# Optimization experiments

Measured on AMD Instinct MI355X. Metric: run time of the kernel, lower is better.

Reference implementation:

```python
import jax, jax.numpy as jnp
import numpy as np

N = 50000

def _norm_coeffs(edge_index, n):
    # add self-loops, compute symmetric GCN normalization D^-1/2 (A+I) D^-1/2
    loops = jnp.arange(n, dtype=edge_index.dtype)
    src = jnp.concatenate([edge_index[0], loops])
    dst = jnp.concatenate([edge_index[1], loops])
    deg = jax.ops.segment_sum(jnp.ones_like(dst, dtype=jnp.float32), dst, num_segments=n)
    dinv = jnp.where(deg > 0, jax.lax.rsqrt(deg), 0.0)
    norm = dinv[src] * dinv[dst]  # [E+N]
    return src, dst, norm

def _gcn(x, W, b, src, dst, norm, n):
    h = x @ W                                   # [N, out]
    m = h[src] * norm[:, None]                  # [E+N, out] gather + scale
    return jax.ops.segment_sum(m, dst, num_segments=n) + b

def setup_inputs() -> dict:
    key = jax.random.key(0)
    ks = jax.random.split(key, 8)
    d, h = 96, 96
    E = 800000
    return {
        "x": jax.random.normal(ks[0], (N, d), jnp.float32),
        "edge_index": jax.random.randint(ks[1], (2, E), 0, N, dtype=jnp.int64),
        "h_prev": jax.random.normal(ks[2], (N, h), jnp.float32),
        "Wx": jax.random.normal(ks[3], (d, h), jnp.float32) * (1.0 / np.sqrt(d)),
        "bx": jnp.zeros((h,), jnp.float32),
        "Wuh": jax.random.normal(ks[4], (2 * h, h), jnp.float32) * (1.0 / np.sqrt(2 * h)),
        "buh": jnp.zeros((h,), jnp.float32),
        "Wch": jax.random.normal(ks[5], (2 * h, h), jnp.float32) * (1.0 / np.sqrt(2 * h)),
        "bch": jnp.zeros((h,), jnp.float32),
    }

def reference(x, edge_index, h_prev, Wx, bx, Wuh, buh, Wch, bch):
    n = x.shape[0]
    src, dst, norm = _norm_coeffs(edge_index, n)
    x_gcn = _gcn(x, Wx, bx, src, dst, norm, n)
    combined = jnp.concatenate([x_gcn, h_prev], axis=1)
    # original computes gcn_uh(combined) twice for u and r; identical math -> compute once
    g = jax.nn.sigmoid(_gcn(combined, Wuh, buh, src, dst, norm, n))
    u = g
    r = g
    combined_r = jnp.concatenate([x_gcn, r * h_prev], axis=1)
    c = jnp.tanh(_gcn(combined_r, Wch, bch, src, dst, norm, n))
    return u * h_prev + (1.0 - u) * c
```

## Files before the change

kernel.cpp:

```cpp
#include <hip/hip_runtime.h>
#include <hip/hip_bf16.h>

#define D 96
#define CAP 64
typedef long long i64;
typedef unsigned short u16;

typedef __bf16 bf16x8 __attribute__((ext_vector_type(8)));
typedef float f32x16 __attribute__((ext_vector_type(16)));

__device__ __forceinline__ float bf2f(u16 u) {
  union { unsigned u; float f; } x; x.u = ((unsigned)u) << 16; return x.f;
}
__device__ __forceinline__ void unpack8(uint4 p, float* a) {
  a[0] = bf2f((u16)(p.x & 0xffff)); a[1] = bf2f((u16)(p.x >> 16));
  a[2] = bf2f((u16)(p.y & 0xffff)); a[3] = bf2f((u16)(p.y >> 16));
  a[4] = bf2f((u16)(p.z & 0xffff)); a[5] = bf2f((u16)(p.z >> 16));
  a[6] = bf2f((u16)(p.w & 0xffff)); a[7] = bf2f((u16)(p.w >> 16));
}

__device__ __forceinline__ void split8(const float* v8, bf16x8& hi, bf16x8& lo) {
  unsigned hu[4], lu[4];
#pragma unroll
  for (int p = 0; p < 4; p++) {
    float v0 = v8[2 * p], v1 = v8[2 * p + 1];
    unsigned u0 = __float_as_uint(v0), u1 = __float_as_uint(v1);
    hu[p] = (u0 >> 16) | (u1 & 0xffff0000u);
    float l0 = v0 - __uint_as_float(u0 & 0xffff0000u);
    float l1 = v1 - __uint_as_float(u1 & 0xffff0000u);
    lu[p] = (__float_as_uint(l0) >> 16) | (__float_as_uint(l1) & 0xffff0000u);
  }
  union { uint4 q; bf16x8 v; } H, L;
  H.q = make_uint4(hu[0], hu[1], hu[2], hu[3]);
  L.q = make_uint4(lu[0], lu[1], lu[2], lu[3]);
  hi = H.v; lo = L.v;
}

__global__ __launch_bounds__(256) void k_detect(const unsigned* __restrict__ w,
                                                int* flag, int E) {
  if (threadIdx.x < 64) {
    int lane = threadIdx.x;
    int lim = (E < 2048) ? E : 2048;
    unsigned acc = 0;
    for (int j = lane; j < lim; j += 64) acc |= w[2 * j + 1];
#pragma unroll
    for (int off = 32; off > 0; off >>= 1) acc |= __shfl_down(acc, off, 64);
    if (lane == 0) *flag = (acc == 0) ? 1 : 0;
  }
}

__global__ __launch_bounds__(256) void k_wprep(const float* __restrict__ Wx,
                                               const float* __restrict__ Wuh,
                                               const float* __restrict__ Wch,
                                               u16* __restrict__ wxh, u16* __restrict__ wxl,
                                               u16* __restrict__ wuhh, u16* __restrict__ wuhl,
                                               u16* __restrict__ wchh, u16* __restrict__ wchl) {
  int cid = blockIdx.x * 256 + threadIdx.x;
  const float* W; u16 *oh, *ol; int loc;
  if (cid < 1152) { W = Wx; oh = wxh; ol = wxl; loc = cid; }
  else if (cid < 3456) { W = Wuh; oh = wuhh; ol = wuhl; loc = cid - 1152; }
  else if (cid < 5760) { W = Wch; oh = wchh; ol = wchl; loc = cid - 3456; }
  else return;
  int oct = loc / 96;
  int j = loc - oct * 96;
  int k0 = oct * 8;
  unsigned hu[4], lu[4];
#pragma unroll
  for (int p = 0; p < 4; p++) {
    float v0 = W[(size_t)(k0 + 2 * p) * D + j];
    float v1 = W[(size_t)(k0 + 2 * p + 1) * D + j];
    unsigned u0 = __float_as_uint(v0), u1 = __float_as_uint(v1);
    hu[p] = (u0 >> 16) | (u1 & 0xffff0000u);
    float l0 = v0 - __uint_as_float(u0 & 0xffff0000u);
    float l1 = v1 - __uint_as_float(u1 & 0xffff0000u);
    lu[p] = (__float_as_uint(l0) >> 16) | (__float_as_uint(l1) & 0xffff0000u);
  }
  *(uint4*)&oh[(size_t)loc * 8] = make_uint4(hu[0], hu[1], hu[2], hu[3]);
  *(uint4*)&ol[(size_t)loc * 8] = make_uint4(lu[0], lu[1], lu[2], lu[3]);
}

__global__ __launch_bounds__(256) void k_bucket(const int* __restrict__ e32,
                                                const i64* __restrict__ e64,
                                                const int* __restrict__ flagp,
                                                uint2* __restrict__ region,
                                                int* __restrict__ cntmat,
                                                int E, int N, int NB) {
  __shared__ int lofs[256];
  const int tid = threadIdx.x;
  const int blk = blockIdx.x;
  lofs[tid] = 0;
  __syncthreads();
  const int f = *flagp;
  const int chunk = (E + gridDim.x - 1) / gridDim.x;
  const int lo = blk * chunk;
  const int hi = min(E, lo + chunk);
  for (int i = lo + tid; i < hi; i += 256) {
    int d, s;
    if (f) { d = (int)e64[(size_t)E + i]; s = (int)e64[i]; }
    else   { d = e32[(size_t)E + i];      s = e32[i]; }
    if ((unsigned)d >= (unsigned)N || (unsigned)s >= (unsigned)N) continue;
    int q = d >> 8;
    int r = atomicAdd(&lofs[q], 1);
    if (r < CAP)
      region[((size_t)q * 256 + blk) * CAP + r] = make_uint2((unsigned)s, (unsigned)d);
  }
  __syncthreads();
  if (tid < NB) cntmat[blk * 256 + tid] = min(lofs[tid], CAP);
}

__global__ __launch_bounds__(256) void k_csr(const uint2* __restrict__ region,
                                             const int* __restrict__ cntmat,
                                             int* __restrict__ deg,
                                             int* __restrict__ csrp, int NB) {
  __shared__ int ldeg[256];
  __shared__ int lcsr[256 * CAP];
  const int tid = threadIdx.x;
  const int b = blockIdx.x;
  ldeg[tid] = 0;
  __syncthreads();
  int cnt = cntmat[tid * 256 + b];
  const uint2* cell = region + ((size_t)b * 256 + tid) * CAP;
  for (int k = 0; k < cnt; k++) {
    uint2 e = cell[k];
    int node = (int)(e.y & 255u);
    int r = atomicAdd(&ldeg[node], 1);
    if (r < CAP) lcsr[node * CAP + r] = (int)e.x;
  }
  __syncthreads();
  deg[(b << 8) + tid] = ldeg[tid];
  const uint4* src = (const uint4*)lcsr;
  uint4* dst = (uint4*)(csrp + ((size_t)b << 8) * CAP);
#pragma unroll
  for (int it = 0; it < (256 * CAP) / 4 / 256; it++)
    dst[tid + it * 256] = src[tid + it * 256];
}

template <int KTOT, int MODE>
__global__ __launch_bounds__(256) void gemm_mfma(
    const float* __restrict__ xin, const float* __restrict__ xg,
    const float* __restrict__ hprev, const float* __restrict__ gmul,
    const u16* __restrict__ whi, const u16* __restrict__ wlo,
    const int* __restrict__ deg, __hip_bfloat16* __restrict__ t, int N) {
  const int l = threadIdx.x & 63;
  const int wave = threadIdx.x >> 6;
  const int lr = l & 31;
  const int kg = l >> 5;
  const int rb = blockIdx.x * 128 + wave * 32;
  const int row = rb + lr;
  const bool rok = row < N;
  constexpr int steps = KTOT / 16;

  f32x16 acc0, acc1, acc2;
#pragma unroll
  for (int i = 0; i < 16; i++) { acc0[i] = 0.f; acc1[i] = 0.f; acc2[i] = 0.f; }

  auto loadA = [&](int s, float4& va, float4& vb, float4& ga, float4& gb) {
    if (!rok) return;
    int k0 = s * 16 + kg * 8;
    if (MODE == 0) {
      const float* src = &xin[(size_t)row * D + k0];
      va = *(const float4*)src; vb = *(const float4*)(src + 4);
    } else if (s < 6) {
      const float* src = &xg[(size_t)row * D + k0];
      va = *(const float4*)src; vb = *(const float4*)(src + 4);
    } else {
      const float* src = &hprev[(size_t)row * D + (k0 - 96)];
      va = *(const float4*)src; vb = *(const float4*)(src + 4);
      if (MODE == 2) {
        const float* gs = &gmul[(size_t)row * D + (k0 - 96)];
        ga = *(const float4*)gs; gb = *(const float4*)(gs + 4);
      }
    }
  };

  auto computeS = [&](int s, float4 va, float4 vb, float4 ga, float4 gb) {
    if (MODE == 2 && s >= 6) {
      va.x *= ga.x; va.y *= ga.y; va.z *= ga.z; va.w *= ga.w;
      vb.x *= gb.x; vb.y *= gb.y; vb.z *= gb.z; vb.w *= gb.w;
    }
    float a8[8] = {va.x, va.y, va.z, va.w, vb.x, vb.y, vb.z, vb.w};
    bf16x8 ah, al;
    split8(a8, ah, al);
    const size_t wbase = ((size_t)(s * 2 + kg) * 96 + lr) * 8;
    union { uint4 q; bf16x8 v; } B0h, B1h, B2h, B0l, B1l, B2l;
    B0h.q = *(const uint4*)&whi[wbase];
    B1h.q = *(const uint4*)&whi[wbase + 32 * 8];
    B2h.q = *(const uint4*)&whi[wbase + 64 * 8];
    B0l.q = *(const uint4*)&wlo[wbase];
    B1l.q = *(const uint4*)&wlo[wbase + 32 * 8];
    B2l.q = *(const uint4*)&wlo[wbase + 64 * 8];
    acc0 = __builtin_amdgcn_mfma_f32_32x32x16_bf16(ah, B0h.v, acc0, 0, 0, 0);
    acc1 = __builtin_amdgcn_mfma_f32_32x32x16_bf16(ah, B1h.v, acc1, 0, 0, 0);
    acc2 = __builtin_amdgcn_mfma_f32_32x32x16_bf16(ah, B2h.v, acc2, 0, 0, 0);
    acc0 = __builtin_amdgcn_mfma_f32_32x32x16_bf16(al, B0h.v, acc0, 0, 0, 0);
    acc1 = __builtin_amdgcn_mfma_f32_32x32x16_bf16(al, B1h.v, acc1, 0, 0, 0);
    acc2 = __builtin_amdgcn_mfma_f32_32x32x16_bf16(al, B2h.v, acc2, 0, 0, 0);
    acc0 = __builtin_amdgcn_mfma_f32_32x32x16_bf16(ah, B0l.v, acc0, 0, 0, 0);
    acc1 = __builtin_amdgcn_mfma_f32_32x32x16_bf16(ah, B1l.v, acc1, 0, 0, 0);
    acc2 = __builtin_amdgcn_mfma_f32_32x32x16_bf16(ah, B2l.v, acc2, 0, 0, 0);
  };

  float4 z4 = make_float4(0.f, 0.f, 0.f, 0.f);
  float4 va0 = z4, vb0 = z4, ga0 = z4, gb0 = z4;
  float4 va1 = z4, vb1 = z4, ga1 = z4, gb1 = z4;
  loadA(0, va0, vb0, ga0, gb0);
  loadA(1, va1, vb1, ga1, gb1);
#pragma unroll 1
  for (int s = 0; s < steps; s += 2) {
    computeS(s, va0, vb0, ga0, gb0);
    if (s + 2 < steps) loadA(s + 2, va0, vb0, ga0, gb0);
    computeS(s + 1, va1, vb1, ga1, gb1);
    if (s + 3 < steps) loadA(s + 3, va1, vb1, ga1, gb1);
  }

  const int rbase = rb + 4 * kg;
#pragma unroll
  for (int r = 0; r < 16; r++) {
    int orow = rbase + (r & 3) + 8 * (r >> 2);
    if (orow >= N) continue;
    float dv = rsqrtf((float)deg[orow] + 1.0f);
    __hip_bfloat16* tp = &t[(size_t)orow * D];
    tp[lr]      = __float2bfloat16(acc0[r] * dv);
    tp[lr + 32] = __float2bfloat16(acc1[r] * dv);
    tp[lr + 64] = __float2bfloat16(acc2[r] * dv);
  }
}

template <int MODE>
__global__ __launch_bounds__(192) void gather_fin(
    const __hip_bfloat16* __restrict__ t, const int* __restrict__ deg,
    const int* __restrict__ csrp,
    const float* __restrict__ bias,
    const float* __restrict__ g, const float* __restrict__ hprev,
    float* __restrict__ outf, int N) {
  __shared__ int lidx[16 * 65];
  __shared__ int ldeg[16];
  const int tid = threadIdx.x;
  const int vbase = blockIdx.x * 16;
#pragma unroll
  for (int it = 0; it < 6; it++) {
    int i = tid + it * 192;
    if (i < 1024) {
      int n = i >> 6, j = i & 63;
      lidx[n * 65 + j] = csrp[((size_t)(vbase + n)) * CAP + j];
    }
  }
  if (tid < 16) ldeg[tid] = deg[vbase + tid];
  __syncthreads();
  const int n = tid / 12;
  const int c8 = tid - n * 12;
  const int v = vbase + n;
  if (v >= N) return;
  const uint4* t8 = (const uint4*)t;
  float acc[8];
  unpack8(t8[(size_t)v * 12 + c8], acc);
  int dv_i = ldeg[n];
  int nb = min(dv_i, CAP);
  const int* ip = &lidx[n * 65];
  int j = 0;
  for (; j + 8 <= nb; j += 8) {
    int s0 = ip[j],     s1 = ip[j + 1], s2 = ip[j + 2], s3 = ip[j + 3];
    int s4 = ip[j + 4], s5 = ip[j + 5], s6 = ip[j + 6], s7 = ip[j + 7];
    uint4 p0 = t8[(size_t)s0 * 12 + c8];
    uint4 p1 = t8[(size_t)s1 * 12 + c8];
    uint4 p2 = t8[(size_t)s2 * 12 + c8];
    uint4 p3 = t8[(size_t)s3 * 12 + c8];
    uint4 p4 = t8[(size_t)s4 * 12 + c8];
    uint4 p5 = t8[(size_t)s5 * 12 + c8];
    uint4 p6 = t8[(size_t)s6 * 12 + c8];
    uint4 p7 = t8[(size_t)s7 * 12 + c8];
    float a0[8], a1[8], a2[8], a3[8], a4[8], a5[8], a6[8], a7[8];
    unpack8(p0, a0); unpack8(p1, a1); unpack8(p2, a2); unpack8(p3, a3);
    unpack8(p4, a4); unpack8(p5, a5); unpack8(p6, a6); unpack8(p7, a7);
#pragma unroll
    for (int q = 0; q < 8; q++)
      acc[q] += ((a0[q] + a1[q]) + (a2[q] + a3[q])) + ((a4[q] + a5[q]) + (a6[q] + a7[q]));
  }
  for (; j + 4 <= nb; j += 4) {
    int s0 = ip[j], s1 = ip[j + 1], s2 = ip[j + 2], s3 = ip[j + 3];
    uint4 p0 = t8[(size_t)s0 * 12 + c8];
    uint4 p1 = t8[(size_t)s1 * 12 + c8];
    uint4 p2 = t8[(size_t)s2 * 12 + c8];
    uint4 p3 = t8[(size_t)s3 * 12 + c8];
    float a0[8], a1[8], a2[8], a3[8];
    unpack8(p0, a0); unpack8(p1, a1); unpack8(p2, a2); unpack8(p3, a3);
#pragma unroll
    for (int q = 0; q < 8; q++) acc[q] += (a0[q] + a1[q]) + (a2[q] + a3[q]);
  }
  for (; j < nb; j++) {
    int s = ip[j];
    float a0[8];
    unpack8(t8[(size_t)s * 12 + c8], a0);
#pragma unroll
    for (int q = 0; q < 8; q++) acc[q] += a0[q];
  }
  float dv = rsqrtf((float)dv_i + 1.0f);
  float4 bA = ((const float4*)bias)[c8 * 2];
  float4 bB = ((const float4*)bias)[c8 * 2 + 1];
  float z[8] = {dv * acc[0] + bA.x, dv * acc[1] + bA.y, dv * acc[2] + bA.z, dv * acc[3] + bA.w,
                dv * acc[4] + bB.x, dv * acc[5] + bB.y, dv * acc[6] + bB.z, dv * acc[7] + bB.w};
  const size_t oidx = (size_t)v * 12 + c8;
  float4 oA, oB;
  if (MODE == 1) {
    oA = make_float4(z[0], z[1], z[2], z[3]);
    oB = make_float4(z[4], z[5], z[6], z[7]);
  } else if (MODE == 2) {
    oA = make_float4(1.0f / (1.0f + expf(-z[0])), 1.0f / (1.0f + expf(-z[1])),
                     1.0f / (1.0f + expf(-z[2])), 1.0f / (1.0f + expf(-z[3])));
    oB = make_float4(1.0f / (1.0f + expf(-z[4])), 1.0f / (1.0f + expf(-z[5])),
                     1.0f / (1.0f + expf(-z[6])), 1.0f / (1.0f + expf(-z[7])));
  } else {
    float4 uA = ((const float4*)g)[oidx * 2], uB = ((const float4*)g)[oidx * 2 + 1];
    float4 hA = ((const float4*)hprev)[oidx * 2], hB = ((const float4*)hprev)[oidx * 2 + 1];
    oA = make_float4(uA.x * hA.x + (1.0f - uA.x) * tanhf(z[0]),
                     uA.y * hA.y + (1.0f - uA.y) * tanhf(z[1]),
                     uA.z * hA.z + (1.0f - uA.z) * tanhf(z[2]),
                     uA.w * hA.w + (1.0f - uA.w) * tanhf(z[3]));
    oB = make_float4(uB.x * hB.x + (1.0f - uB.x) * tanhf(z[4]),
                     uB.y * hB.y + (1.0f - uB.y) * tanhf(z[5]),
                     uB.z * hB.z + (1.0f - uB.z) * tanhf(z[6]),
                     uB.w * hB.w + (1.0f - uB.w) * tanhf(z[7]));
  }
  ((float4*)outf)[oidx * 2] = oA;
  ((float4*)outf)[oidx * 2 + 1] = oB;
}

extern "C" void kernel_launch(void* const* d_in, const int* in_sizes, int n_in,
                              void* d_out, int out_size, void* d_ws, size_t ws_size,
                              hipStream_t stream) {
  const float* x = (const float*)d_in[0];
  const int* ei32 = (const int*)d_in[1];
  const i64* ei64 = (const i64*)d_in[1];
  const unsigned* eiw = (const unsigned*)d_in[1];
  const float* hp = (const float*)d_in[2];
  const float* Wx = (const float*)d_in[3];
  const float* bx = (const float*)d_in[4];
  const float* Wuh = (const float*)d_in[5];
  const float* buh = (const float*)d_in[6];
  const float* Wch = (const float*)d_in[7];
  const float* bch = (const float*)d_in[8];
  float* out = (float*)d_out;

  const int N = in_sizes[0] / D;
  const int E = in_sizes[1] / 2;
  const size_t NF = (size_t)N * D;
  const int NB = (N + 255) >> 8;
  const int R = NB << 8;

  char* base = (char*)d_ws;
  int* flag = (int*)base;
  u16* wxh = (u16*)(base + 256);
  u16* wxl = wxh + 9216;
  u16* wuhh = wxl + 9216;
  u16* wuhl = wuhh + 18432;
  u16* wchh = wuhl + 18432;
  u16* wchl = wchh + 18432;
  int* deg = (int*)(wchl + 18432);
  int* cntmat = deg + R;
  uint2* region = (uint2*)(cntmat + 65536);
  int* csrp = (int*)(region + (size_t)NB * 256 * CAP);
  __hip_bfloat16* t = (__hip_bfloat16*)(csrp + (size_t)R * CAP);
  float* xg = (float*)((char*)t + NF * 2);
  float* g = xg + NF;

  const int gb = (N + 127) / 128;
  const int fb = (N + 15) / 16;

  k_detect<<<1, 256, 0, stream>>>(eiw, flag, E);
  k_wprep<<<23, 256, 0, stream>>>(Wx, Wuh, Wch, wxh, wxl, wuhh, wuhl, wchh, wchl);
  k_bucket<<<256, 256, 0, stream>>>(ei32, ei64, flag, region, cntmat, E, N, NB);
  k_csr<<<NB, 256, 0, stream>>>(region, cntmat, deg, csrp, NB);

  gemm_mfma<96, 0><<<gb, 256, 0, stream>>>(x, nullptr, nullptr, nullptr, wxh, wxl, deg, t, N);
  gather_fin<1><<<fb, 192, 0, stream>>>(t, deg, csrp, bx, nullptr, nullptr, xg, N);

  gemm_mfma<192, 1><<<gb, 256, 0, stream>>>(nullptr, xg, hp, nullptr, wuhh, wuhl, deg, t, N);
  gather_fin<2><<<fb, 192, 0, stream>>>(t, deg, csrp, buh, nullptr, nullptr, g, N);

  gemm_mfma<192, 2><<<gb, 256, 0, stream>>>(nullptr, xg, hp, g, wchh, wchl, deg, t, N);
  gather_fin<3><<<fb, 192, 0, stream>>>(t, deg, csrp, bch, g, hp, out, N);
}
```

Before: 294.5 us.

## Switch GEMM to 16x16x32 MFMA tiles with two-wave split-K reduction

The dense GEMM kernels move from 32x32x16 MFMA tiles to 16x16x32 MFMA tiles, so each wave covers 16 rows and all 96 output columns. For the K=192 GEMMs, the two waves of a 128-thread block each take half of K (x_gcn or h_prev) and combine partial sums through a small shared-memory buffer. For K=96, each wave handles its own 16 rows. This launches many more, smaller blocks to raise occupancy and spread memory traffic. In exchange it adds a barrier and LDS round trip, and each block reuses the weight loads less.

```diff
diff --git a/kernel.cpp b/kernel.cpp
--- a/kernel.cpp
+++ b/kernel.cpp
@@ -7,7 +7,7 @@
 typedef unsigned short u16;
 
 typedef __bf16 bf16x8 __attribute__((ext_vector_type(8)));
-typedef float f32x16 __attribute__((ext_vector_type(16)));
+typedef float f32x4 __attribute__((ext_vector_type(4)));
 
 __device__ __forceinline__ float bf2f(u16 u) {
   union { unsigned u; float f; } x; x.u = ((unsigned)u) << 16; return x.f;
@@ -136,93 +136,100 @@
 }
 
 template <int KTOT, int MODE>
-__global__ __launch_bounds__(256) void gemm_mfma(
+__global__ __launch_bounds__(128) void gemm_mfma(
     const float* __restrict__ xin, const float* __restrict__ xg,
     const float* __restrict__ hprev, const float* __restrict__ gmul,
     const u16* __restrict__ whi, const u16* __restrict__ wlo,
     const int* __restrict__ deg, __hip_bfloat16* __restrict__ t, int N) {
+  constexpr bool KS = (KTOT == 192);
+  __shared__ float lcomb[64][25];
   const int l = threadIdx.x & 63;
-  const int wave = threadIdx.x >> 6;
-  const int lr = l & 31;
-  const int kg = l >> 5;
-  const int rb = blockIdx.x * 128 + wave * 32;
-  const int row = rb + lr;
+  const int wv = threadIdx.x >> 6;
+  const int j16 = l & 15;
+  const int koct = l >> 4;
+  const int rb = KS ? blockIdx.x * 16 : blockIdx.x * 32 + wv * 16;
+  const int row = rb + j16;
   const bool rok = row < N;
-  constexpr int steps = KTOT / 16;
-
-  f32x16 acc0, acc1, acc2;
-#pragma unroll
-  for (int i = 0; i < 16; i++) { acc0[i] = 0.f; acc1[i] = 0.f; acc2[i] = 0.f; }
-
-  auto loadA = [&](int s, float4& va, float4& vb, float4& ga, float4& gb) {
-    if (!rok) return;
-    int k0 = s * 16 + kg * 8;
-    if (MODE == 0) {
-      const float* src = &xin[(size_t)row * D + k0];
-      va = *(const float4*)src; vb = *(const float4*)(src + 4);
-    } else if (s < 6) {
-      const float* src = &xg[(size_t)row * D + k0];
-      va = *(const float4*)src; vb = *(const float4*)(src + 4);
-    } else {
-      const float* src = &hprev[(size_t)row * D + (k0 - 96)];
-      va = *(const float4*)src; vb = *(const float4*)(src + 4);
-      if (MODE == 2) {
-        const float* gs = &gmul[(size_t)row * D + (k0 - 96)];
-        ga = *(const float4*)gs; gb = *(const float4*)(gs + 4);
+
+  f32x4 c0, c1, c2, c3, c4, c5;
+#pragma unroll
+  for (int i = 0; i < 4; i++) { c0[i] = 0.f; c1[i] = 0.f; c2[i] = 0.f;
+                                c3[i] = 0.f; c4[i] = 0.f; c5[i] = 0.f; }
+
+#define COLT(CT, ACC) do {                                                  \
+    union { uint4 q; bf16x8 v; } Bh, Bl;                                    \
+    const size_t wb = (so + (CT)*16 + j16) * 8;                             \
+    Bh.q = *(const uint4*)&whi[wb];                                         \
+    Bl.q = *(const uint4*)&wlo[wb];                                         \
+    ACC = __builtin_amdgcn_mfma_f32_16x16x32_bf16(ah, Bh.v, ACC, 0, 0, 0);  \
+    ACC = __builtin_amdgcn_mfma_f32_16x16x32_bf16(al, Bh.v, ACC, 0, 0, 0);  \
+    ACC = __builtin_amdgcn_mfma_f32_16x16x32_bf16(ah, Bl.v, ACC, 0, 0, 0);  \
+  } while (0)
+
+#pragma unroll
+  for (int ss = 0; ss < 3; ss++) {
+    const int s = KS ? (wv * 3 + ss) : ss;
+    float a8[8] = {0.f, 0.f, 0.f, 0.f, 0.f, 0.f, 0.f, 0.f};
+    if (rok) {
+      const int kb = ss * 32 + koct * 8;
+      const float* src;
+      if (MODE == 0) src = xin;
+      else if (!KS || wv == 0) src = xg;
+      else src = hprev;
+      float4 va = *(const float4*)&src[(size_t)row * D + kb];
+      float4 vb = *(const float4*)&src[(size_t)row * D + kb + 4];
+      if (MODE == 2 && KS && wv == 1) {
+        float4 ga = *(const float4*)&gmul[(size_t)row * D + kb];
+        float4 gb = *(const float4*)&gmul[(size_t)row * D + kb + 4];
+        va.x *= ga.x; va.y *= ga.y; va.z *= ga.z; va.w *= ga.w;
+        vb.x *= gb.x; vb.y *= gb.y; vb.z *= gb.z; vb.w *= gb.w;
+      }
+      a8[0] = va.x; a8[1] = va.y; a8[2] = va.z; a8[3] = va.w;
+      a8[4] = vb.x; a8[5] = vb.y; a8[6] = vb.z; a8[7] = vb.w;
+    }
+    bf16x8 ah, al;
+    split8(a8, ah, al);
+    const size_t so = (size_t)(s * 4 + koct) * 96;
+    COLT(0, c0); COLT(1, c1); COLT(2, c2);
+    COLT(3, c3); COLT(4, c4); COLT(5, c5);
+  }
+#undef COLT
+
+  if (KS) {
+    if (wv == 1) {
+#pragma unroll
+      for (int r = 0; r < 4; r++) {
+        lcomb[l][0 + r]  = c0[r]; lcomb[l][4 + r]  = c1[r];
+        lcomb[l][8 + r]  = c2[r]; lcomb[l][12 + r] = c3[r];
+        lcomb[l][16 + r] = c4[r]; lcomb[l][20 + r] = c5[r];
       }
     }
-  };
-
-  auto computeS = [&](int s, float4 va, float4 vb, float4 ga, float4 gb) {
-    if (MODE == 2 && s >= 6) {
-      va.x *= ga.x; va.y *= ga.y; va.z *= ga.z; va.w *= ga.w;
-      vb.x *= gb.x; vb.y *= gb.y; vb.z *= gb.z; vb.w *= gb.w;
+    __syncthreads();
+    if (wv == 1) return;
+#pragma unroll
+    for (int r = 0; r < 4; r++) {
+      c0[r] += lcomb[l][0 + r];  c1[r] += lcomb[l][4 + r];
+      c2[r] += lcomb[l][8 + r];  c3[r] += lcomb[l][12 + r];
+      c4[r] += lcomb[l][16 + r]; c5[r] += lcomb[l][20 + r];
     }
-    float a8[8] = {va.x, va.y, va.z, va.w, vb.x, vb.y, vb.z, vb.w};
-    bf16x8 ah, al;
-    split8(a8, ah, al);
-    const size_t wbase = ((size_t)(s * 2 + kg) * 96 + lr) * 8;
-    union { uint4 q; bf16x8 v; } B0h, B1h, B2h, B0l, B1l, B2l;
-    B0h.q = *(const uint4*)&whi[wbase];
-    B1h.q = *(const uint4*)&whi[wbase + 32 * 8];
-    B2h.q = *(const uint4*)&whi[wbase + 64 * 8];
-    B0l.q = *(const uint4*)&wlo[wbase];
-    B1l.q = *(const uint4*)&wlo[wbase + 32 * 8];
-    B2l.q = *(const uint4*)&wlo[wbase + 64 * 8];
-    acc0 = __builtin_amdgcn_mfma_f32_32x32x16_bf16(ah, B0h.v, acc0, 0, 0, 0);
-    acc1 = __builtin_amdgcn_mfma_f32_32x32x16_bf16(ah, B1h.v, acc1, 0, 0, 0);
-    acc2 = __builtin_amdgcn_mfma_f32_32x32x16_bf16(ah, B2h.v, acc2, 0, 0, 0);
-    acc0 = __builtin_amdgcn_mfma_f32_32x32x16_bf16(al, B0h.v, acc0, 0, 0, 0);
-    acc1 = __builtin_amdgcn_mfma_f32_32x32x16_bf16(al, B1h.v, acc1, 0, 0, 0);
-    acc2 = __builtin_amdgcn_mfma_f32_32x32x16_bf16(al, B2h.v, acc2, 0, 0, 0);
-    acc0 = __builtin_amdgcn_mfma_f32_32x32x16_bf16(ah, B0l.v, acc0, 0, 0, 0);
-    acc1 = __builtin_amdgcn_mfma_f32_32x32x16_bf16(ah, B1l.v, acc1, 0, 0, 0);
-    acc2 = __builtin_amdgcn_mfma_f32_32x32x16_bf16(ah, B2l.v, acc2, 0, 0, 0);
-  };
-
-  float4 z4 = make_float4(0.f, 0.f, 0.f, 0.f);
-  float4 va0 = z4, vb0 = z4, ga0 = z4, gb0 = z4;
-  float4 va1 = z4, vb1 = z4, ga1 = z4, gb1 = z4;
-  loadA(0, va0, vb0, ga0, gb0);
-  loadA(1, va1, vb1, ga1, gb1);
-#pragma unroll 1
-  for (int s = 0; s < steps; s += 2) {
-    computeS(s, va0, vb0, ga0, gb0);
-    if (s + 2 < steps) loadA(s + 2, va0, vb0, ga0, gb0);
-    computeS(s + 1, va1, vb1, ga1, gb1);
-    if (s + 3 < steps) loadA(s + 3, va1, vb1, ga1, gb1);
-  }
-
-  const int rbase = rb + 4 * kg;
-#pragma unroll
-  for (int r = 0; r < 16; r++) {
-    int orow = rbase + (r & 3) + 8 * (r >> 2);
+  }
+
+  const int r0 = rb + koct * 4;
+  float dv[4];
+#pragma unroll
+  for (int r = 0; r < 4; r++)
+    dv[r] = (r0 + r < N) ? rsqrtf((float)deg[r0 + r] + 1.0f) : 0.f;
+#pragma unroll
+  for (int r = 0; r < 4; r++) {
+    int orow = r0 + r;
     if (orow >= N) continue;
-    float dv = rsqrtf((float)deg[orow] + 1.0f);
-    __hip_bfloat16* tp = &t[(size_t)orow * D];
-    tp[lr]      = __float2bfloat16(acc0[r] * dv);
-    tp[lr + 32] = __float2bfloat16(acc1[r] * dv);
-    tp[lr + 64] = __float2bfloat16(acc2[r] * dv);
+    __hip_bfloat16* tp = &t[(size_t)orow * D + j16];
+    tp[0]  = __float2bfloat16(c0[r] * dv[r]);
+    tp[16] = __float2bfloat16(c1[r] * dv[r]);
+    tp[32] = __float2bfloat16(c2[r] * dv[r]);
+    tp[48] = __float2bfloat16(c3[r] * dv[r]);
+    tp[64] = __float2bfloat16(c4[r] * dv[r]);
+    tp[80] = __float2bfloat16(c5[r] * dv[r]);
   }
 }
 
@@ -363,7 +370,8 @@
   float* xg = (float*)((char*)t + NF * 2);
   float* g = xg + NF;
 
-  const int gb = (N + 127) / 128;
+  const int gb16 = (N + 15) / 16;
+  const int gb32 = (N + 31) / 32;
   const int fb = (N + 15) / 16;
 
   k_detect<<<1, 256, 0, stream>>>(eiw, flag, E);
@@ -371,12 +379,12 @@
   k_bucket<<<256, 256, 0, stream>>>(ei32, ei64, flag, region, cntmat, E, N, NB);
   k_csr<<<NB, 256, 0, stream>>>(region, cntmat, deg, csrp, NB);
 
-  gemm_mfma<96, 0><<<gb, 256, 0, stream>>>(x, nullptr, nullptr, nullptr, wxh, wxl, deg, t, N);
+  gemm_mfma<96, 0><<<gb32, 128, 0, stream>>>(x, nullptr, nullptr, nullptr, wxh, wxl, deg, t, N);
   gather_fin<1><<<fb, 192, 0, stream>>>(t, deg, csrp, bx, nullptr, nullptr, xg, N);
 
-  gemm_mfma<192, 1><<<gb, 256, 0, stream>>>(nullptr, xg, hp, nullptr, wuhh, wuhl, deg, t, N);
+  gemm_mfma<192, 1><<<gb16, 128, 0, stream>>>(nullptr, xg, hp, nullptr, wuhh, wuhl, deg, t, N);
   gather_fin<2><<<fb, 192, 0, stream>>>(t, deg, csrp, buh, nullptr, nullptr, g, N);
 
-  gemm_mfma<192, 2><<<gb, 256, 0, stream>>>(nullptr, xg, hp, g, wchh, wchl, deg, t, N);
+  gemm_mfma<192, 2><<<gb16, 128, 0, stream>>>(nullptr, xg, hp, g, wchh, wchl, deg, t, N);
   gather_fin<3><<<fb, 192, 0, stream>>>(t, deg, csrp, bch, g, hp, out, N);
 }
```

Result: faster. 264.7 us (-10.1%).
